# Kernel tuning notes

Measured on AMD Instinct MI355X. Metric: run time of the kernel, lower is better.

## Reference

```python
import jax, jax.numpy as jnp
import numpy as np

B, T = 256, 256
INIT_DIM, C_IN, HID, OUT = 128, 64, 512, 10
H = 8
D = HID // H          # head_dim = 64
FF = 4 * HID          # transformer FF dim


def _ln(x, g, b, eps=1e-5):
    m = jnp.mean(x, axis=-1, keepdims=True)
    v = jnp.var(x, axis=-1, keepdims=True)
    return (x - m) * jax.lax.rsqrt(v + eps) * g + b


def _kv(x, Wip, bip, g_in, b_in, Wk, bk, Wv, bv):
    """Hebb vector field projections: x (..., C_IN) -> k,v (..., H, D)."""
    h = _ln(x @ Wip.T + bip, g_in, b_in)                       # (..., HID)
    k = jax.nn.softmax((h @ Wk.T + bk).reshape(*h.shape[:-1], H, D), axis=-1)
    v = (h @ Wv.T + bv).reshape(*h.shape[:-1], H, D)
    return k, v


def setup_inputs() -> dict:
    key = jax.random.key(0)
    ks = jax.random.split(key, 16)
    p = lambda k, shape: jax.random.normal(k, shape, dtype=jnp.float32) * 0.02
    return {
        "initial": jax.random.normal(ks[0], (B, INIT_DIM), dtype=jnp.float32),
        "logsig": jax.random.normal(ks[1], (B, T, C_IN), dtype=jnp.float32),
        # initial_network: initial_dim -> input_channels
        "Wi": p(ks[2], (C_IN, INIT_DIM)), "bi": jnp.zeros((C_IN,), jnp.float32),
        # update_net.input_proj + input_layer_norm
        "Wip": p(ks[3], (HID, C_IN)), "bip": jnp.zeros((HID,), jnp.float32),
        "g_in": jnp.ones((HID,), jnp.float32), "b_in": jnp.zeros((HID,), jnp.float32),
        # key / value nets of the Hebb field
        "Wk": p(ks[4], (HID, HID)), "bk": jnp.zeros((HID,), jnp.float32),
        "Wv": p(ks[5], (HID, HID)), "bv": jnp.zeros((HID,), jnp.float32),
        # query_net, out_proj
        "Wq": p(ks[6], (HID, HID)), "bq": jnp.zeros((HID,), jnp.float32),
        "Wo": p(ks[7], (HID, HID)), "bo": jnp.zeros((HID,), jnp.float32),
        # TransformerFFlayers: LN -> W1 -> relu -> W2, residual
        "g_ff": jnp.ones((HID,), jnp.float32), "b_ff": jnp.zeros((HID,), jnp.float32),
        "W1": p(ks[8], (FF, HID)), "b1": jnp.zeros((FF,), jnp.float32),
        "W2": p(ks[9], (HID, FF)), "b2": jnp.zeros((HID,), jnp.float32),
        # final_linear
        "Wf": p(ks[10], (OUT, HID)), "bf": jnp.zeros((OUT,), jnp.float32),
    }


def reference(initial, logsig, Wi, bi, Wip, bip, g_in, b_in, Wk, bk, Wv, bv,
              Wq, bq, Wo, bo, g_ff, b_ff, W1, b1, W2, b2, Wf, bf):
    # z0 from the initial observation
    init_proj = initial @ Wi.T + bi                             # (B, C_IN)
    k0, v0 = _kv(init_proj, Wip, bip, g_in, b_in, Wk, bk, Wv, bv)
    z0 = jnp.einsum('bhd,bhe->bhde', v0, k0)                    # (B,H,D,D)

    # Hebb field over all control steps (field independent of z).
    ks_, vs_ = _kv(logsig, Wip, bip, g_in, b_in, Wk, bk, Wv, bv)  # (B,T,H,D)
    # RK4, step=1, floor-indexed control x(t)=logsig[:,floor(t)]:
    # step n adds (5*F[n] + F[n+1]) / 6  =>  total weights [5/6, 1,...,1, 1/6]
    w = jnp.ones((T,), dtype=logsig.dtype).at[0].set(5.0 / 6.0).at[-1].set(1.0 / 6.0)
    z_t = z0 + jnp.einsum('t,bthd,bthe->bhde', w, vs_, ks_)     # (B,H,D,D)

    # query readout from the last control step
    hq = _ln(logsig[:, -1] @ Wip.T + bip, g_in, b_in)           # (B, HID)
    q = jax.nn.softmax((hq @ Wq.T + bq).reshape(B, H, D), axis=-1)
    y = jnp.einsum('bhde,bhe->bhd', z_t, q).reshape(B, HID)

    y = y @ Wo.T + bo
    # transformer FF block with residual
    hff = _ln(y, g_ff, b_ff)
    y = y + (jax.nn.relu(hff @ W1.T + b1) @ W2.T + b2)
    return y @ Wf.T + bf                                        # (B, OUT)
```

## Files before the change

### kernel.cpp

```cpp
#include <hip/hip_runtime.h>
#include <hip/hip_bf16.h>
#include <math.h>

#define B_ 256
#define T_ 256
#define CIN 64
#define HID 512
#define NH 8
#define HD 64
#define FFD 2048
#define OUTD 10

typedef __bf16 bf16x8 __attribute__((ext_vector_type(8)));
typedef float f32x4 __attribute__((ext_vector_type(4)));

#define HSOFF(r,c) (((r)<<10) + ((((c)<<1)) ^ ((((r)&7))<<4)))
#define HS2OFF(r,c) (((r)<<12) + ((((c)<<1)) ^ ((((r)&7))<<4)))

__device__ __forceinline__ float bf2f(unsigned u){
  union { unsigned i; float f; } c; c.i = u << 16; return c.f;
}
__device__ __forceinline__ unsigned pk2(float a, float b){
  return ((unsigned)__bfloat16_as_ushort(__float2bfloat16(a))) |
         (((unsigned)__bfloat16_as_ushort(__float2bfloat16(b))) << 16);
}

__device__ __forceinline__ void pack_one(const float* __restrict__ W,
                                         __hip_bfloat16* __restrict__ P,
                                         const int K, int g){
  int row = g / (K/8), kg = g % (K/8);
  int k0 = kg*8;
  int n0 = row >> 6, j = (row >> 4) & 3, lr = row & 15;
  int s = k0 >> 5, lg = (k0 >> 3) & 3;
  int lane = lg*16 + lr;
  const float* src = W + (size_t)row*K + k0;
  float4 a = *(const float4*)src;
  float4 b = *(const float4*)(src+4);
  uint4 p = { pk2(a.x,a.y), pk2(a.z,a.w), pk2(b.x,b.y), pk2(b.z,b.w) };
  size_t off = ((((size_t)n0*(K>>5) + s)*4 + j)*64 + lane)*8;
  *(uint4*)(P + off) = p;
}

#define G_KV (HID*HID/8)
#define G_FF (FFD*HID/8)
#define G_IP (HID*CIN/8)
#define G_I  (CIN*128/8)
#define PK_TOT (4*G_KV + 2*G_FF + G_IP + G_I)
__global__ __launch_bounds__(256) void k_pack(
    const float* __restrict__ Wk, const float* __restrict__ Wv,
    const float* __restrict__ Wo, const float* __restrict__ Wq,
    const float* __restrict__ W1, const float* __restrict__ W2,
    const float* __restrict__ Wip, const float* __restrict__ Wi,
    __hip_bfloat16* __restrict__ Pk, __hip_bfloat16* __restrict__ Pv,
    __hip_bfloat16* __restrict__ Po, __hip_bfloat16* __restrict__ Pq,
    __hip_bfloat16* __restrict__ P1, __hip_bfloat16* __restrict__ P2,
    __hip_bfloat16* __restrict__ Pip, __hip_bfloat16* __restrict__ Pi)
{
  int g = blockIdx.x*256 + threadIdx.x;
  if (g < G_KV) { pack_one(Wk, Pk, HID, g); return; }  g -= G_KV;
  if (g < G_KV) { pack_one(Wv, Pv, HID, g); return; }  g -= G_KV;
  if (g < G_KV) { pack_one(Wo, Po, HID, g); return; }  g -= G_KV;
  if (g < G_KV) { pack_one(Wq, Pq, HID, g); return; }  g -= G_KV;
  if (g < G_FF) { pack_one(W1, P1, HID, g); return; }  g -= G_FF;
  if (g < G_FF) { pack_one(W2, P2, FFD, g); return; }  g -= G_FF;
  if (g < G_IP) { pack_one(Wip, Pip, CIN, g); return; }  g -= G_IP;
  if (g < G_I ) { pack_one(Wi, Pi, 128, g); }
}

__device__ __forceinline__ void proj_ln(
    char* Hs, const __hip_bfloat16* __restrict__ Pip,
    const float* __restrict__ bip, const float* __restrict__ g_in,
    const float* __restrict__ b_in,
    float (*red)[8][2], float (*ms2)[2],
    int tid, int w, int l, int lr, int lg)
{
  f32x4 acc[4][4];
  #pragma unroll
  for (int i=0;i<4;i++)
    #pragma unroll
    for (int j=0;j<4;j++) acc[i][j] = (f32x4){0.f,0.f,0.f,0.f};
  #pragma unroll
  for (int s = 0; s < 2; s++){
    bf16x8 af[4], bfr[4];
    #pragma unroll
    for (int i=0;i<4;i++)
      af[i] = *(const bf16x8*)(Hs + HSOFF(i*16 + lr, s*32 + lg*8));
    const __hip_bfloat16* fb = Pip + ((size_t)(w*2 + s)*4)*512 + l*8;
    #pragma unroll
    for (int j=0;j<4;j++)
      bfr[j] = *(const bf16x8*)(fb + j*512);
    #pragma unroll
    for (int i=0;i<4;i++)
      #pragma unroll
      for (int j=0;j<4;j++)
        acc[i][j] = __builtin_amdgcn_mfma_f32_16x16x32_bf16(af[i], bfr[j], acc[i][j], 0,0,0);
  }
  float bipv[4], gv[4], bbv[4];
  #pragma unroll
  for (int j=0;j<4;j++){
    int col = w*64 + j*16 + lr;
    bipv[j] = bip[col]; gv[j] = g_in[col]; bbv[j] = b_in[col];
  }
  #pragma unroll
  for (int i=0;i<4;i++){
    #pragma unroll
    for (int r=0;r<4;r++){
      float s = 0.f, s2 = 0.f;
      #pragma unroll
      for (int j=0;j<4;j++){ float v = acc[i][j][r] + bipv[j]; s += v; s2 += v*v; }
      #pragma unroll
      for (int o=1;o<16;o<<=1){ s += __shfl_xor(s,o); s2 += __shfl_xor(s2,o); }
      if (lr == 0){ int row = i*16 + lg*4 + r; red[row][w][0] = s; red[row][w][1] = s2; }
    }
  }
  __syncthreads();
  if (tid < 64){
    float S = 0.f, S2 = 0.f;
    #pragma unroll
    for (int k=0;k<8;k++){ S += red[tid][k][0]; S2 += red[tid][k][1]; }
    float m = S*(1.f/512.f), var = S2*(1.f/512.f) - m*m;
    ms2[tid][0] = m; ms2[tid][1] = rsqrtf(var + 1e-5f);
  }
  __syncthreads();
  #pragma unroll
  for (int i=0;i<4;i++){
    #pragma unroll
    for (int r=0;r<4;r++){
      int row = i*16 + lg*4 + r;
      float m = ms2[row][0], rs = ms2[row][1];
      #pragma unroll
      for (int j=0;j<4;j++){
        int col = w*64 + j*16 + lr;
        float v = (acc[i][j][r] + bipv[j] - m)*rs*gv[j] + bbv[j];
        *(unsigned short*)(Hs + HSOFF(row, col)) =
            __bfloat16_as_ushort(__float2bfloat16(v));
      }
    }
  }
  __syncthreads();
}

__device__ __forceinline__ void gemm512_pk(
    const char* Hs, const __hip_bfloat16* __restrict__ Pm,
    f32x4 acc[4][4], int l, int lr, int lg)
{
  #pragma unroll
  for (int i=0;i<4;i++)
    #pragma unroll
    for (int j=0;j<4;j++) acc[i][j] = (f32x4){0.f,0.f,0.f,0.f};
  #pragma unroll
  for (int s = 0; s < 16; s++){
    bf16x8 af[4], bfr[4];
    #pragma unroll
    for (int i=0;i<4;i++)
      af[i] = *(const bf16x8*)(Hs + HSOFF(i*16 + lr, s*32 + lg*8));
    const __hip_bfloat16* fb = Pm + (size_t)s*2048 + l*8;
    #pragma unroll
    for (int j=0;j<4;j++)
      bfr[j] = *(const bf16x8*)(fb + j*512);
    #pragma unroll
    for (int i=0;i<4;i++)
      #pragma unroll
      for (int j=0;j<4;j++)
        acc[i][j] = __builtin_amdgcn_mfma_f32_16x16x32_bf16(af[i], bfr[j], acc[i][j], 0,0,0);
  }
}

__device__ __forceinline__ void proj_ln16(
    char* Hs, const __hip_bfloat16* __restrict__ Pip,
    const float* __restrict__ bip, const float* __restrict__ g_in,
    const float* __restrict__ b_in,
    float (*red)[8][2], float (*ms2)[2],
    int tid, int w, int l, int lr, int lg)
{
  f32x4 acc[4];
  #pragma unroll
  for (int j=0;j<4;j++) acc[j] = (f32x4){0.f,0.f,0.f,0.f};
  #pragma unroll
  for (int s = 0; s < 2; s++){
    bf16x8 af = *(const bf16x8*)(Hs + HSOFF(lr, s*32 + lg*8));
    const __hip_bfloat16* fb = Pip + ((size_t)(w*2 + s)*4)*512 + l*8;
    #pragma unroll
    for (int j=0;j<4;j++){
      bf16x8 bfr = *(const bf16x8*)(fb + j*512);
      acc[j] = __builtin_amdgcn_mfma_f32_16x16x32_bf16(af, bfr, acc[j], 0,0,0);
    }
  }
  float bipv[4], gv[4], bbv[4];
  #pragma unroll
  for (int j=0;j<4;j++){
    int col = w*64 + j*16 + lr;
    bipv[j] = bip[col]; gv[j] = g_in[col]; bbv[j] = b_in[col];
  }
  #pragma unroll
  for (int r=0;r<4;r++){
    float s = 0.f, s2 = 0.f;
    #pragma unroll
    for (int j=0;j<4;j++){ float v = acc[j][r] + bipv[j]; s += v; s2 += v*v; }
    #pragma unroll
    for (int o=1;o<16;o<<=1){ s += __shfl_xor(s,o); s2 += __shfl_xor(s2,o); }
    if (lr == 0){ int row = lg*4 + r; red[row][w][0] = s; red[row][w][1] = s2; }
  }
  __syncthreads();
  if (tid < 16){
    float S = 0.f, S2 = 0.f;
    #pragma unroll
    for (int k=0;k<8;k++){ S += red[tid][k][0]; S2 += red[tid][k][1]; }
    float m = S*(1.f/512.f), var = S2*(1.f/512.f) - m*m;
    ms2[tid][0] = m; ms2[tid][1] = rsqrtf(var + 1e-5f);
  }
  __syncthreads();
  #pragma unroll
  for (int r=0;r<4;r++){
    int row = lg*4 + r;
    float m = ms2[row][0], rs = ms2[row][1];
    #pragma unroll
    for (int j=0;j<4;j++){
      int col = w*64 + j*16 + lr;
      float v = (acc[j][r] + bipv[j] - m)*rs*gv[j] + bbv[j];
      *(unsigned short*)(Hs + HSOFF(row, col)) =
          __bfloat16_as_ushort(__float2bfloat16(v));
    }
  }
  __syncthreads();
}

__device__ __forceinline__ void gemm512_pk16(
    const char* Hs, const __hip_bfloat16* __restrict__ Pm,
    f32x4 acc[4], int l, int lr, int lg)
{
  #pragma unroll
  for (int j=0;j<4;j++) acc[j] = (f32x4){0.f,0.f,0.f,0.f};
  #pragma unroll
  for (int s = 0; s < 16; s++){
    bf16x8 af = *(const bf16x8*)(Hs + HSOFF(lr, s*32 + lg*8));
    const __hip_bfloat16* fb = Pm + (size_t)s*2048 + l*8;
    #pragma unroll
    for (int j=0;j<4;j++){
      bf16x8 bfr = *(const bf16x8*)(fb + j*512);
      acc[j] = __builtin_amdgcn_mfma_f32_16x16x32_bf16(af, bfr, acc[j], 0,0,0);
    }
  }
}

__global__ __launch_bounds__(512) void k_pre(
    const float* __restrict__ initial, const float* __restrict__ logsig,
    const __hip_bfloat16* __restrict__ Pi,  const float* __restrict__ bi,
    const __hip_bfloat16* __restrict__ Pip, const float* __restrict__ bip,
    const float* __restrict__ g_in, const float* __restrict__ b_in,
    const __hip_bfloat16* __restrict__ Pq, const float* __restrict__ bq,
    const __hip_bfloat16* __restrict__ Pk, const float* __restrict__ bk,
    const __hip_bfloat16* __restrict__ Pv, const float* __restrict__ bv,
    float* __restrict__ qout, float* __restrict__ yinit)
{
  int b0 = blockIdx.x*16;
  int tid = threadIdx.x;
  int w = tid >> 6, l = tid & 63, lr = l & 15, lg = l >> 4;
  __shared__ __align__(16) char Hs[16*1024];
  __shared__ float red[16][8][2];
  __shared__ float ms2[16][2];
  __shared__ float salS[16][8];
  f32x4 acc[4];

  {
    int row = tid >> 5, c = (tid & 31)*2;
    const float* s = logsig + ((size_t)(b0+row)*T_ + (T_-1))*CIN + c;
    float2 a = *(const float2*)s;
    *(unsigned*)(Hs + HSOFF(row, c)) = pk2(a.x, a.y);
  }
  __syncthreads();
  proj_ln16(Hs, Pip, bip, g_in, b_in, red, ms2, tid, w, l, lr, lg);

  float qreg[4][4];
  gemm512_pk16(Hs, Pq + (size_t)w*32768, acc, l, lr, lg);
  {
    float bqv[4];
    #pragma unroll
    for (int j=0;j<4;j++) bqv[j] = bq[w*64 + j*16 + lr];
    #pragma unroll
    for (int r=0;r<4;r++){
      float v0 = acc[0][r]+bqv[0], v1 = acc[1][r]+bqv[1];
      float v2 = acc[2][r]+bqv[2], v3 = acc[3][r]+bqv[3];
      float mx = fmaxf(fmaxf(v0,v1),fmaxf(v2,v3));
      #pragma unroll
      for (int o=1;o<16;o<<=1) mx = fmaxf(mx, __shfl_xor(mx,o));
      float e0=__expf(v0-mx), e1=__expf(v1-mx), e2=__expf(v2-mx), e3=__expf(v3-mx);
      float se = e0+e1+e2+e3;
      #pragma unroll
      for (int o=1;o<16;o<<=1) se += __shfl_xor(se,o);
      float inv = 1.f/se;
      qreg[0][r]=e0*inv; qreg[1][r]=e1*inv; qreg[2][r]=e2*inv; qreg[3][r]=e3*inv;
      int row = lg*4 + r;
      size_t base = (size_t)(b0+row)*HID + w*64 + lr;
      qout[base +  0] = qreg[0][r]; qout[base + 16] = qreg[1][r];
      qout[base + 32] = qreg[2][r]; qout[base + 48] = qreg[3][r];
    }
  }
  __syncthreads();

  {
    int row = tid >> 5, c = (tid & 31)*4;
    const float* s = initial + (size_t)(b0+row)*128 + c;
    float4 a = *(const float4*)s;
    uint2 p = { pk2(a.x,a.y), pk2(a.z,a.w) };
    *(uint2*)(Hs + HSOFF(row, 64 + c)) = p;
  }
  __syncthreads();
  if (w < 4){
    f32x4 a2 = (f32x4){0.f,0.f,0.f,0.f};
    #pragma unroll
    for (int s = 0; s < 4; s++){
      bf16x8 af = *(const bf16x8*)(Hs + HSOFF(lr, 64 + s*32 + lg*8));
      bf16x8 bfr = *(const bf16x8*)(Pi + ((size_t)s*4 + w)*512 + l*8);
      a2 = __builtin_amdgcn_mfma_f32_16x16x32_bf16(af, bfr, a2, 0,0,0);
    }
    float bic = bi[w*16 + lr];
    #pragma unroll
    for (int r=0;r<4;r++){
      *(unsigned short*)(Hs + HSOFF(lg*4 + r, w*16 + lr)) =
          __bfloat16_as_ushort(__float2bfloat16(a2[r] + bic));
    }
  }
  __syncthreads();

  proj_ln16(Hs, Pip, bip, g_in, b_in, red, ms2, tid, w, l, lr, lg);

  gemm512_pk16(Hs, Pk + (size_t)w*32768, acc, l, lr, lg);
  {
    float bkv[4];
    #pragma unroll
    for (int j=0;j<4;j++) bkv[j] = bk[w*64 + j*16 + lr];
    #pragma unroll
    for (int r=0;r<4;r++){
      float v0 = acc[0][r]+bkv[0], v1 = acc[1][r]+bkv[1];
      float v2 = acc[2][r]+bkv[2], v3 = acc[3][r]+bkv[3];
      float mx = fmaxf(fmaxf(v0,v1),fmaxf(v2,v3));
      #pragma unroll
      for (int o=1;o<16;o<<=1) mx = fmaxf(mx, __shfl_xor(mx,o));
      float e0=__expf(v0-mx), e1=__expf(v1-mx), e2=__expf(v2-mx), e3=__expf(v3-mx);
      float se = e0+e1+e2+e3;
      float sq = e0*qreg[0][r]+e1*qreg[1][r]+e2*qreg[2][r]+e3*qreg[3][r];
      #pragma unroll
      for (int o=1;o<16;o<<=1){ se += __shfl_xor(se,o); sq += __shfl_xor(sq,o); }
      if (lr == 0) salS[lg*4 + r][w] = sq/se;
    }
  }
  __syncthreads();

  gemm512_pk16(Hs, Pv + (size_t)w*32768, acc, l, lr, lg);
  {
    float bvv[4];
    #pragma unroll
    for (int j=0;j<4;j++) bvv[j] = bv[w*64 + j*16 + lr];
    #pragma unroll
    for (int r=0;r<4;r++){
      int row = lg*4 + r;
      float s = salS[row][w];
      size_t base = (size_t)(b0+row)*HID + w*64 + lr;
      yinit[base +  0] = s*(acc[0][r]+bvv[0]);
      yinit[base + 16] = s*(acc[1][r]+bvv[1]);
      yinit[base + 32] = s*(acc[2][r]+bvv[2]);
      yinit[base + 48] = s*(acc[3][r]+bvv[3]);
    }
  }
}

__global__ __launch_bounds__(512, 4) void k_fused(
    const float* __restrict__ logsig,
    const __hip_bfloat16* __restrict__ Pip,
    const float* __restrict__ bip,
    const float* __restrict__ g_in, const float* __restrict__ b_in,
    const __hip_bfloat16* __restrict__ Pk,
    const float* __restrict__ bk,
    const float* __restrict__ qws,
    float* __restrict__ up,
    float* __restrict__ Asp)
{
  int b = blockIdx.x, tc = blockIdx.y;
  int tid = threadIdx.x;
  int w = tid >> 6, l = tid & 63, lr = l & 15, lg = l >> 4;
  __shared__ __align__(16) char Hs[64*1024];
  __shared__ float red[64][8][2];
  __shared__ float ms2[64][2];
  __shared__ float als[64][8];
  __shared__ unsigned short als_bt[2][16][64];

  {
    int row = tid >> 3, cc = (tid & 7)*8;
    const float* srow = logsig + ((size_t)b*T_ + tc*64 + row)*CIN + cc;
    float4 a = *(const float4*)(srow);
    float4 c = *(const float4*)(srow+4);
    uint4 p = { pk2(a.x,a.y), pk2(a.z,a.w), pk2(c.x,c.y), pk2(c.z,c.w) };
    *(uint4*)(Hs + HSOFF(row, cc)) = p;
  }
  __syncthreads();

  proj_ln(Hs, Pip, bip, g_in, b_in, red, ms2, tid, w, l, lr, lg);

  f32x4 acc[4][4];
  gemm512_pk(Hs, Pk + (size_t)w*32768, acc, l, lr, lg);

  {
    float bkv[4], qv[4];
    #pragma unroll
    for (int j=0;j<4;j++){
      bkv[j] = bk[w*64 + j*16 + lr];
      qv[j]  = qws[(size_t)b*HID + w*64 + j*16 + lr];
    }
    #pragma unroll
    for (int i=0;i<4;i++){
      #pragma unroll
      for (int r=0;r<4;r++){
        float v0 = acc[i][0][r]+bkv[0], v1 = acc[i][1][r]+bkv[1];
        float v2 = acc[i][2][r]+bkv[2], v3 = acc[i][3][r]+bkv[3];
        float mx = fmaxf(fmaxf(v0,v1),fmaxf(v2,v3));
        #pragma unroll
        for (int o=1;o<16;o<<=1) mx = fmaxf(mx, __shfl_xor(mx,o));
        float e0=__expf(v0-mx), e1=__expf(v1-mx), e2=__expf(v2-mx), e3=__expf(v3-mx);
        float se = e0+e1+e2+e3;
        float sq = e0*qv[0]+e1*qv[1]+e2*qv[2]+e3*qv[3];
        #pragma unroll
        for (int o=1;o<16;o<<=1){ se += __shfl_xor(se,o); sq += __shfl_xor(sq,o); }
        if (lr == 0){
          int row = i*16 + lg*4 + r;
          int t = tc*64 + row;
          float wt = (t == 0) ? (5.f/6.f) : ((t == T_-1) ? (1.f/6.f) : 1.f);
          float alpha = wt * sq / se;
          als[row][w] = alpha;
          __hip_bfloat16 ah = __float2bfloat16(alpha);
          float rem = alpha - __bfloat162float(ah);
          als_bt[0][w][row] = __bfloat16_as_ushort(ah);
          als_bt[1][w][row] = __bfloat16_as_ushort(__float2bfloat16(rem));
        }
      }
    }
  }
  __syncthreads();

  {
    f32x4 uacc[4];
    #pragma unroll
    for (int t=0;t<4;t++) uacc[t] = (f32x4){0.f,0.f,0.f,0.f};
    #pragma unroll
    for (int ks=0; ks<2; ks++){
      bf16x8 afh = *(const bf16x8*)&als_bt[0][lr][ks*32 + lg*8];
      bf16x8 afl = *(const bf16x8*)&als_bt[1][lr][ks*32 + lg*8];
      #pragma unroll
      for (int t=0;t<4;t++){
        int col = w*64 + t*16 + lr;
        int r0 = ks*32 + lg*8;
        uint4 bbu;
        {
          unsigned lo0 = *(const unsigned short*)(Hs + HSOFF(r0,   col));
          unsigned hi0 = *(const unsigned short*)(Hs + HSOFF(r0+1, col));
          unsigned lo1 = *(const unsigned short*)(Hs + HSOFF(r0+2, col));
          unsigned hi1 = *(const unsigned short*)(Hs + HSOFF(r0+3, col));
          unsigned lo2 = *(const unsigned short*)(Hs + HSOFF(r0+4, col));
          unsigned hi2 = *(const unsigned short*)(Hs + HSOFF(r0+5, col));
          unsigned lo3 = *(const unsigned short*)(Hs + HSOFF(r0+6, col));
          unsigned hi3 = *(const unsigned short*)(Hs + HSOFF(r0+7, col));
          bbu.x = lo0 | (hi0 << 16);
          bbu.y = lo1 | (hi1 << 16);
          bbu.z = lo2 | (hi2 << 16);
          bbu.w = lo3 | (hi3 << 16);
        }
        bf16x8 bvv = __builtin_bit_cast(bf16x8, bbu);
        uacc[t] = __builtin_amdgcn_mfma_f32_16x16x32_bf16(afh, bvv, uacc[t], 0,0,0);
        uacc[t] = __builtin_amdgcn_mfma_f32_16x16x32_bf16(afl, bvv, uacc[t], 0,0,0);
      }
    }
    if (lg < 2){
      #pragma unroll
      for (int t=0;t<4;t++){
        #pragma unroll
        for (int rr=0; rr<4; rr++){
          int h = lg*4 + rr;
          up[((((size_t)b*NH + h)*4 + tc)*HID) + w*64 + t*16 + lr] = uacc[t][rr];
        }
      }
    }
    float s = als[l][w];
    #pragma unroll
    for (int o=1;o<64;o<<=1) s += __shfl_xor(s,o);
    if (l == 0) Asp[(((size_t)b*NH + w)*4) + tc] = s;
  }
}

__global__ __launch_bounds__(256) void k_ured(
    const float* __restrict__ up, const float* __restrict__ Asp,
    __hip_bfloat16* __restrict__ u_bf, float* __restrict__ Asum)
{
  int bh = blockIdx.x, tid = threadIdx.x;
  size_t base = (size_t)bh*4*HID;
  float s0 = 0.f, s1 = 0.f;
  #pragma unroll
  for (int c=0;c<4;c++){
    s0 += up[base + (size_t)c*HID + 2*tid];
    s1 += up[base + (size_t)c*HID + 2*tid+1];
  }
  ((unsigned*)u_bf)[(size_t)bh*(HID/2) + tid] = pk2(s0, s1);
  if (tid == 0)
    Asum[bh] = Asp[(size_t)bh*4] + Asp[(size_t)bh*4+1] + Asp[(size_t)bh*4+2] + Asp[(size_t)bh*4+3];
}

__global__ __launch_bounds__(512) void k_tail(
    const __hip_bfloat16* __restrict__ u_bf,
    const __hip_bfloat16* __restrict__ Pv,
    const float* __restrict__ bv, const float* __restrict__ Asum,
    const float* __restrict__ yinit,
    const __hip_bfloat16* __restrict__ Po, const float* __restrict__ bo,
    const float* __restrict__ g_ff, const float* __restrict__ b_ff,
    const __hip_bfloat16* __restrict__ P1, const float* __restrict__ b1,
    const __hip_bfloat16* __restrict__ P2, const float* __restrict__ b2,
    const float* __restrict__ Wf, const float* __restrict__ bfv,
    float* __restrict__ out)
{
  int b0 = blockIdx.x*16;
  int tid = threadIdx.x;
  int w = tid >> 6, l = tid & 63, lr = l & 15, lg = l >> 4;
  __shared__ __align__(16) char Hs[16*1024];
  __shared__ __align__(16) char A1[16*4096];
  __shared__ float yoS[16][516];
  __shared__ float red[16][8][2];
  __shared__ float ms2[16][2];
  f32x4 acc[4];

  #pragma unroll
  for (int j=0;j<4;j++) acc[j] = (f32x4){0.f,0.f,0.f,0.f};
  #pragma unroll
  for (int s = 0; s < 16; s++){
    bf16x8 af = *(const bf16x8*)(u_bf + ((size_t)(b0 + lr)*NH + w)*HID + s*32 + lg*8);
    const __hip_bfloat16* fb = Pv + (size_t)w*32768 + (size_t)s*2048 + l*8;
    #pragma unroll
    for (int j=0;j<4;j++){
      bf16x8 bfr = *(const bf16x8*)(fb + j*512);
      acc[j] = __builtin_amdgcn_mfma_f32_16x16x32_bf16(af, bfr, acc[j], 0,0,0);
    }
  }
  {
    float bvv[4];
    #pragma unroll
    for (int j=0;j<4;j++) bvv[j] = bv[w*64 + j*16 + lr];
    #pragma unroll
    for (int r=0;r<4;r++){
      int row = lg*4 + r;
      float As = Asum[(size_t)(b0+row)*NH + w];
      #pragma unroll
      for (int j=0;j<4;j++){
        int col = w*64 + j*16 + lr;
        float v = acc[j][r] + yinit[(size_t)(b0+row)*HID + col] + bvv[j]*As;
        *(unsigned short*)(Hs + HSOFF(row, col)) =
            __bfloat16_as_ushort(__float2bfloat16(v));
      }
    }
  }
  __syncthreads();

  gemm512_pk16(Hs, Po + (size_t)w*32768, acc, l, lr, lg);
  {
    float bov[4], gv[4], bbv[4];
    #pragma unroll
    for (int j=0;j<4;j++){
      int col = w*64 + j*16 + lr;
      bov[j] = bo[col]; gv[j] = g_ff[col]; bbv[j] = b_ff[col];
    }
    #pragma unroll
    for (int r=0;r<4;r++){
      int row = lg*4 + r;
      float s = 0.f, s2 = 0.f;
      #pragma unroll
      for (int j=0;j<4;j++){
        float v = acc[j][r] + bov[j];
        yoS[row][w*64 + j*16 + lr] = v;
        s += v; s2 += v*v;
      }
      #pragma unroll
      for (int o=1;o<16;o<<=1){ s += __shfl_xor(s,o); s2 += __shfl_xor(s2,o); }
      if (lr == 0){ red[row][w][0] = s; red[row][w][1] = s2; }
    }
    __syncthreads();
    if (tid < 16){
      float S = 0.f, S2 = 0.f;
      #pragma unroll
      for (int k=0;k<8;k++){ S += red[tid][k][0]; S2 += red[tid][k][1]; }
      float m = S*(1.f/512.f), var = S2*(1.f/512.f) - m*m;
      ms2[tid][0] = m; ms2[tid][1] = rsqrtf(var + 1e-5f);
    }
    __syncthreads();
    #pragma unroll
    for (int r=0;r<4;r++){
      int row = lg*4 + r;
      float m = ms2[row][0], rs = ms2[row][1];
      #pragma unroll
      for (int j=0;j<4;j++){
        int col = w*64 + j*16 + lr;
        float v = (yoS[row][col] - m)*rs*gv[j] + bbv[j];
        *(unsigned short*)(Hs + HSOFF(row, col)) =
            __bfloat16_as_ushort(__float2bfloat16(v));
      }
    }
  }
  __syncthreads();

  #pragma unroll
  for (int n0 = 0; n0 < 4; n0++){
    gemm512_pk16(Hs, P1 + (size_t)(w*4 + n0)*32768, acc, l, lr, lg);
    #pragma unroll
    for (int j=0;j<4;j++){
      int col = (w*4 + n0)*64 + j*16 + lr;
      float bc = b1[col];
      #pragma unroll
      for (int r=0;r<4;r++){
        int row = lg*4 + r;
        *(unsigned short*)(A1 + HS2OFF(row, col)) =
            __bfloat16_as_ushort(__float2bfloat16(fmaxf(acc[j][r] + bc, 0.f)));
      }
    }
  }
  __syncthreads();

  #pragma unroll
  for (int j=0;j<4;j++) acc[j] = (f32x4){0.f,0.f,0.f,0.f};
  #pragma unroll
  for (int s = 0; s < 64; s++){
    bf16x8 af = *(const bf16x8*)(A1 + HS2OFF(lr, s*32 + lg*8));
    const __hip_bfloat16* fb = P2 + (size_t)w*131072 + (size_t)s*2048 + l*8;
    #pragma unroll
    for (int j=0;j<4;j++){
      bf16x8 bfr = *(const bf16x8*)(fb + j*512);
      acc[j] = __builtin_amdgcn_mfma_f32_16x16x32_bf16(af, bfr, acc[j], 0,0,0);
    }
  }
  {
    float b2v[4];
    #pragma unroll
    for (int j=0;j<4;j++) b2v[j] = b2[w*64 + j*16 + lr];
    #pragma unroll
    for (int r=0;r<4;r++){
      int row = lg*4 + r;
      #pragma unroll
      for (int j=0;j<4;j++){
        int col = w*64 + j*16 + lr;
        yoS[row][col] = acc[j][r] + b2v[j] + yoS[row][col];
      }
    }
  }
  __syncthreads();

  {
    int pair = tid >> 1, half = tid & 1;
    if (pair < 16*OUTD){
      int row = pair / OUTD, oc = pair % OUTD;
      const float4* wr = (const float4*)(Wf + (size_t)oc*HID) + half*64;
      float sacc = 0.f;
      #pragma unroll 8
      for (int k4 = 0; k4 < 64; k4++){
        float4 a = wr[k4];
        int c = half*256 + k4*4;
        sacc += a.x*yoS[row][c] + a.y*yoS[row][c+1]
              + a.z*yoS[row][c+2] + a.w*yoS[row][c+3];
      }
      sacc += __shfl_xor(sacc, 1);
      if (half == 0) out[(size_t)(b0+row)*OUTD + oc] = bfv[oc] + sacc;
    }
  }
}

extern "C" void kernel_launch(void* const* d_in, const int* in_sizes, int n_in,
                              void* d_out, int out_size, void* d_ws, size_t ws_size,
                              hipStream_t stream)
{
  const float* initial = (const float*)d_in[0];
  const float* logsig  = (const float*)d_in[1];
  const float* Wi  = (const float*)d_in[2];  const float* bi  = (const float*)d_in[3];
  const float* Wip = (const float*)d_in[4];  const float* bip = (const float*)d_in[5];
  const float* g_in= (const float*)d_in[6];  const float* b_in= (const float*)d_in[7];
  const float* Wk  = (const float*)d_in[8];  const float* bk  = (const float*)d_in[9];
  const float* Wv  = (const float*)d_in[10]; const float* bv  = (const float*)d_in[11];
  const float* Wq  = (const float*)d_in[12]; const float* bq  = (const float*)d_in[13];
  const float* Wo  = (const float*)d_in[14]; const float* bo  = (const float*)d_in[15];
  const float* g_ff= (const float*)d_in[16]; const float* b_ff= (const float*)d_in[17];
  const float* W1  = (const float*)d_in[18]; const float* b1  = (const float*)d_in[19];
  const float* W2  = (const float*)d_in[20]; const float* b2  = (const float*)d_in[21];
  const float* Wf  = (const float*)d_in[22]; const float* bf  = (const float*)d_in[23];
  float* out = (float*)d_out;

  char* ws = (char*)d_ws;
  const size_t MB = 1<<20;
  float* qws   = (float*)(ws);
  float* yinit = (float*)(ws + 512*1024);
  __hip_bfloat16* u_bf = (__hip_bfloat16*)(ws + 3*MB);
  float* Asum  = (float*)(ws + 5*MB);
  __hip_bfloat16* Pk  = (__hip_bfloat16*)(ws + 5*MB + 512*1024);
  __hip_bfloat16* Pv  = (__hip_bfloat16*)(ws + 6*MB);
  __hip_bfloat16* P1  = (__hip_bfloat16*)(ws + 6*MB + 512*1024);
  __hip_bfloat16* P2  = (__hip_bfloat16*)(ws + 8*MB + 512*1024);
  __hip_bfloat16* Po  = (__hip_bfloat16*)(ws + 13*MB);
  __hip_bfloat16* Pip = (__hip_bfloat16*)(ws + 15*MB);
  float* up    = (float*)(ws + 16*MB);
  float* Asp   = (float*)(ws + 33*MB);
  __hip_bfloat16* Pq  = (__hip_bfloat16*)(ws + 34*MB);
  __hip_bfloat16* Pi  = (__hip_bfloat16*)(ws + 35*MB);

  k_pack<<<dim3((PK_TOT + 255)/256), 256, 0, stream>>>(
      Wk, Wv, Wo, Wq, W1, W2, Wip, Wi,
      Pk, Pv, Po, Pq, P1, P2, Pip, Pi);
  k_pre<<<dim3(B_/16), 512, 0, stream>>>(initial, logsig, Pi, bi, Pip, bip,
                                         g_in, b_in, Pq, bq, Pk, bk, Pv, bv,
                                         qws, yinit);
  k_fused<<<dim3(B_, 4), 512, 0, stream>>>(logsig, Pip, bip, g_in, b_in,
                                           Pk, bk, qws, up, Asp);
  k_ured<<<dim3(B_*NH), 256, 0, stream>>>(up, Asp, u_bf, Asum);
  k_tail<<<dim3(B_/16), 512, 0, stream>>>(u_bf, Pv, bv, Asum, yinit,
                                          Po, bo, g_ff, b_ff,
                                          P1, b1, P2, b2, Wf, bf, out);
}
```

Baseline: 188.4 us.

## Split tail FF block across four blocks per batch tile with partial-sum reduction kernel

The tail kernel ran only 16 blocks, each doing the whole Wv/Wo/W1/W2 chain for 16 rows. It now launches 4 blocks per row tile, each computing a quarter of the FF hidden dimension (W1 slice and matching W2 K-slice) and writing fp32 partial W2 outputs. A new kernel sums the partials with the residual and bias, then applies the final linear layer. This gives more parallelism and less shared memory per block, at the cost of redundant Wv/Wo/LN work in each of the 4 blocks, an extra launch and global round-trips for the partials.

```diff
diff --git a/kernel.cpp b/kernel.cpp
--- a/kernel.cpp
+++ b/kernel.cpp
@@ -15,7 +15,6 @@
 typedef float f32x4 __attribute__((ext_vector_type(4)));
 
 #define HSOFF(r,c) (((r)<<10) + ((((c)<<1)) ^ ((((r)&7))<<4)))
-#define HS2OFF(r,c) (((r)<<12) + ((((c)<<1)) ^ ((((r)&7))<<4)))
 
 __device__ __forceinline__ float bf2f(unsigned u){
   union { unsigned i; float f; } c; c.i = u << 16; return c.f;
@@ -503,7 +502,7 @@
     Asum[bh] = Asp[(size_t)bh*4] + Asp[(size_t)bh*4+1] + Asp[(size_t)bh*4+2] + Asp[(size_t)bh*4+3];
 }
 
-__global__ __launch_bounds__(512) void k_tail(
+__global__ __launch_bounds__(512) void k_tail_a(
     const __hip_bfloat16* __restrict__ u_bf,
     const __hip_bfloat16* __restrict__ Pv,
     const float* __restrict__ bv, const float* __restrict__ Asum,
@@ -511,16 +510,16 @@
     const __hip_bfloat16* __restrict__ Po, const float* __restrict__ bo,
     const float* __restrict__ g_ff, const float* __restrict__ b_ff,
     const __hip_bfloat16* __restrict__ P1, const float* __restrict__ b1,
-    const __hip_bfloat16* __restrict__ P2, const float* __restrict__ b2,
-    const float* __restrict__ Wf, const float* __restrict__ bfv,
-    float* __restrict__ out)
+    const __hip_bfloat16* __restrict__ P2,
+    float* __restrict__ yo,
+    float* __restrict__ yp2)
 {
   int b0 = blockIdx.x*16;
+  int qd = blockIdx.y;
   int tid = threadIdx.x;
   int w = tid >> 6, l = tid & 63, lr = l & 15, lg = l >> 4;
   __shared__ __align__(16) char Hs[16*1024];
-  __shared__ __align__(16) char A1[16*4096];
-  __shared__ float yoS[16][516];
+  __shared__ __align__(16) char A1q[16*1024];
   __shared__ float red[16][8][2];
   __shared__ float ms2[16][2];
   f32x4 acc[4];
@@ -571,7 +570,6 @@
       #pragma unroll
       for (int j=0;j<4;j++){
         float v = acc[j][r] + bov[j];
-        yoS[row][w*64 + j*16 + lr] = v;
         s += v; s2 += v*v;
       }
       #pragma unroll
@@ -594,59 +592,63 @@
       #pragma unroll
       for (int j=0;j<4;j++){
         int col = w*64 + j*16 + lr;
-        float v = (yoS[row][col] - m)*rs*gv[j] + bbv[j];
+        float v = acc[j][r] + bov[j];
+        if (qd == 0) yo[(size_t)(b0+row)*HID + col] = v;
         *(unsigned short*)(Hs + HSOFF(row, col)) =
-            __bfloat16_as_ushort(__float2bfloat16(v));
-      }
-    }
-  }
-  __syncthreads();
-
-  #pragma unroll
-  for (int n0 = 0; n0 < 4; n0++){
-    gemm512_pk16(Hs, P1 + (size_t)(w*4 + n0)*32768, acc, l, lr, lg);
+            __bfloat16_as_ushort(__float2bfloat16((v - m)*rs*gv[j] + bbv[j]));
+      }
+    }
+  }
+  __syncthreads();
+
+  gemm512_pk16(Hs, P1 + (size_t)(qd*8 + w)*32768, acc, l, lr, lg);
+  {
     #pragma unroll
     for (int j=0;j<4;j++){
-      int col = (w*4 + n0)*64 + j*16 + lr;
-      float bc = b1[col];
+      int lcol = w*64 + j*16 + lr;
+      float bc = b1[(qd*8 + w)*64 + j*16 + lr];
       #pragma unroll
       for (int r=0;r<4;r++){
         int row = lg*4 + r;
-        *(unsigned short*)(A1 + HS2OFF(row, col)) =
+        *(unsigned short*)(A1q + HSOFF(row, lcol)) =
             __bfloat16_as_ushort(__float2bfloat16(fmaxf(acc[j][r] + bc, 0.f)));
       }
     }
   }
   __syncthreads();
 
-  #pragma unroll
-  for (int j=0;j<4;j++) acc[j] = (f32x4){0.f,0.f,0.f,0.f};
-  #pragma unroll
-  for (int s = 0; s < 64; s++){
-    bf16x8 af = *(const bf16x8*)(A1 + HS2OFF(lr, s*32 + lg*8));
-    const __hip_bfloat16* fb = P2 + (size_t)w*131072 + (size_t)s*2048 + l*8;
-    #pragma unroll
-    for (int j=0;j<4;j++){
-      bf16x8 bfr = *(const bf16x8*)(fb + j*512);
-      acc[j] = __builtin_amdgcn_mfma_f32_16x16x32_bf16(af, bfr, acc[j], 0,0,0);
-    }
-  }
-  {
-    float b2v[4];
-    #pragma unroll
-    for (int j=0;j<4;j++) b2v[j] = b2[w*64 + j*16 + lr];
+  {
+    const __hip_bfloat16* Pm = P2 + ((size_t)(w*64 + qd*16)*4)*512;
+    gemm512_pk16(A1q, Pm, acc, l, lr, lg);
     #pragma unroll
     for (int r=0;r<4;r++){
       int row = lg*4 + r;
       #pragma unroll
       for (int j=0;j<4;j++){
         int col = w*64 + j*16 + lr;
-        yoS[row][col] = acc[j][r] + b2v[j] + yoS[row][col];
-      }
-    }
-  }
-  __syncthreads();
-
+        yp2[((((size_t)blockIdx.x*4 + qd)*16) + row)*HID + col] = acc[j][r];
+      }
+    }
+  }
+}
+
+__global__ __launch_bounds__(512) void k_fin(
+    const float* __restrict__ yo, const float* __restrict__ yp2,
+    const float* __restrict__ b2,
+    const float* __restrict__ Wf, const float* __restrict__ bfv,
+    float* __restrict__ out)
+{
+  int g = blockIdx.x, b0 = g*16;
+  int tid = threadIdx.x;
+  __shared__ float yoS[16][516];
+  for (int i = tid; i < 16*HID; i += 512){
+    int row = i >> 9, col = i & 511;
+    size_t pb = (((size_t)g*4)*16 + row)*HID + col;
+    float v = yo[(size_t)(b0+row)*HID + col] + b2[col]
+            + yp2[pb] + yp2[pb + 16*HID] + yp2[pb + 2*16*HID] + yp2[pb + 3*16*HID];
+    yoS[row][col] = v;
+  }
+  __syncthreads();
   {
     int pair = tid >> 1, half = tid & 1;
     if (pair < 16*OUTD){
@@ -695,12 +697,14 @@
   __hip_bfloat16* Pv  = (__hip_bfloat16*)(ws + 6*MB);
   __hip_bfloat16* P1  = (__hip_bfloat16*)(ws + 6*MB + 512*1024);
   __hip_bfloat16* P2  = (__hip_bfloat16*)(ws + 8*MB + 512*1024);
+  float* yo    = (float*)(ws + 10*MB + 512*1024);
   __hip_bfloat16* Po  = (__hip_bfloat16*)(ws + 13*MB);
   __hip_bfloat16* Pip = (__hip_bfloat16*)(ws + 15*MB);
   float* up    = (float*)(ws + 16*MB);
   float* Asp   = (float*)(ws + 33*MB);
   __hip_bfloat16* Pq  = (__hip_bfloat16*)(ws + 34*MB);
   __hip_bfloat16* Pi  = (__hip_bfloat16*)(ws + 35*MB);
+  float* yp2   = (float*)(ws + 36*MB);
 
   k_pack<<<dim3((PK_TOT + 255)/256), 256, 0, stream>>>(
       Wk, Wv, Wo, Wq, W1, W2, Wip, Wi,
@@ -711,7 +715,8 @@
   k_fused<<<dim3(B_, 4), 512, 0, stream>>>(logsig, Pip, bip, g_in, b_in,
                                            Pk, bk, qws, up, Asp);
   k_ured<<<dim3(B_*NH), 256, 0, stream>>>(up, Asp, u_bf, Asum);
-  k_tail<<<dim3(B_/16), 512, 0, stream>>>(u_bf, Pv, bv, Asum, yinit,
-                                          Po, bo, g_ff, b_ff,
-                                          P1, b1, P2, b2, Wf, bf, out);
-}
+  k_tail_a<<<dim3(B_/16, 4), 512, 0, stream>>>(u_bf, Pv, bv, Asum, yinit,
+                                               Po, bo, g_ff, b_ff,
+                                               P1, b1, P2, yo, yp2);
+  k_fin<<<dim3(B_/16), 512, 0, stream>>>(yo, yp2, b2, Wf, bf, out);
+}
```

Result: faster. 160.5 us (median of 2 runs) (-14.8%).
